# Kernel optimization log

Hardware: AMD Instinct MI355X
Metric: run time of the kernel (lower is better)

Reference implementation:

```python
import jax, jax.numpy as jnp
import numpy as np

N_E = 8192
E_DIM = 256
BETA = 0.25


def setup_inputs() -> dict:
    key = jax.random.key(0)
    k_z, k_w = jax.random.split(key)
    z = jax.random.normal(k_z, (32, E_DIM, 32, 32), dtype=jnp.float32)
    # nn.Embedding weight init: uniform(-1/n_e, 1/n_e)
    W = jax.random.uniform(k_w, (N_E, E_DIM), dtype=jnp.float32,
                           minval=-1.0 / N_E, maxval=1.0 / N_E)
    return {"z": z, "W": W}


def reference(z, W):
    B, C, H, Wd = z.shape
    beta = jnp.float32(BETA)
    z_nhwc = jnp.transpose(z, (0, 2, 3, 1))          # (B,H,W,C)
    zf = z_nhwc.reshape(-1, C)                       # (N,C)
    # squared-distance matrix (N, n_e)
    d = (jnp.sum(zf * zf, axis=1, keepdims=True)
         + jnp.sum(W * W, axis=1)
         - 2.0 * jnp.matmul(zf, W.T))
    idx = jnp.argmin(d, axis=1)                      # (N,)
    # one-hot @ W == gather
    z_q = W[idx].reshape(z_nhwc.shape)               # (B,H,W,C)
    loss = (jnp.mean((jax.lax.stop_gradient(z_q) - z_nhwc) ** 2)
            + beta * jnp.mean((z_q - jax.lax.stop_gradient(z_nhwc)) ** 2))
    # straight-through estimator
    z_q = z_nhwc + jax.lax.stop_gradient(z_q - z_nhwc)
    # codebook usage perplexity
    n = idx.shape[0]
    e_mean = jnp.zeros((N_E,), jnp.float32).at[idx].add(1.0) / n
    perplexity = jnp.exp(-jnp.sum(e_mean * jnp.log(e_mean + 1e-10)))
    z_q = jnp.transpose(z_q, (0, 3, 1, 2))           # back to (B,C,H,W)
    index = idx.reshape(B, H, Wd)
    return z_q, loss, index, perplexity
```

## Files before the change

### kernel.cpp

```cpp
#include <hip/hip_runtime.h>
#include <float.h>
#include <math.h>

#define OUT_LOSS 8388608
#define OUT_IDX  8388609
#define OUT_PERP 8421377

#define WS_ZH    0ull
#define WS_ZL    16777216ull
#define WS_ZT    0ull
#define WS_WH    33554432ull
#define WS_S     37748736ull
#define WS_B     37879808ull
#define WS_MAXW  37912576ull
#define WS_IDX   37912640ull
#define WS_HIST  38043712ull
#define WS_CAND  38076480ull
#define WS_FULL  38469696ull
#define WS_FKEY  38600768ull
#define WS_CNT   38862912ull
#define WS_LOSS  38862920ull

typedef short v8s __attribute__((ext_vector_type(8)));
typedef float v4f __attribute__((ext_vector_type(4)));

__device__ __forceinline__ unsigned short bf16rne(float f) {
  unsigned u = __float_as_uint(f);
  return (unsigned short)((u + 0x7FFFu + ((u >> 16) & 1u)) >> 16);
}
__device__ __forceinline__ float bf16tof(unsigned short h) {
  return __uint_as_float(((unsigned)h) << 16);
}

__device__ __forceinline__ void gl_lds16(const void* g, void* l) {
  __builtin_amdgcn_global_load_lds(
      (const __attribute__((address_space(1))) unsigned int*)g,
      (__attribute__((address_space(3))) unsigned int*)l, 16, 0, 0);
}

__global__ void k_zero(int* __restrict__ hist, unsigned long long* __restrict__ fkey,
                       int* __restrict__ cnt, double* __restrict__ loss,
                       unsigned* __restrict__ maxw) {
  const int i = blockIdx.x * 256 + threadIdx.x;
  if (i < 8192) hist[i] = 0;
  else if (i < 40960) fkey[i - 8192] = ~0ull;
  else if (i == 40960) cnt[0] = 0;
  else if (i == 40961) cnt[1] = 0;
  else if (i == 40962) *loss = 0.0;
  else if (i == 40963) *maxw = 0u;
}

__global__ __launch_bounds__(256) void k_split(const float* __restrict__ W,
                                               unsigned short* __restrict__ Wh) {
  const int u = blockIdx.x * 256 + threadIdx.x;
  const int kc = u >> 15, grp = (u >> 6) & 511, q = (u >> 4) & 3, col = u & 15;
  const int j = grp * 16 + col, k0 = kc * 32 + q * 8;
  const float4 w0 = *(const float4*)(W + (size_t)j * 256 + k0);
  const float4 w1 = *(const float4*)(W + (size_t)j * 256 + k0 + 4);
  const float wv[8] = {w0.x, w0.y, w0.z, w0.w, w1.x, w1.y, w1.z, w1.w};
  unsigned short h[8] __attribute__((aligned(16)));
#pragma unroll
  for (int i = 0; i < 8; ++i) h[i] = bf16rne(wv[i]);
  *(uint4*)(Wh + (size_t)u * 8) = *(const uint4*)h;
}

__global__ __launch_bounds__(256) void k_splitz(const float* __restrict__ z,
    unsigned short* __restrict__ Zh, unsigned short* __restrict__ Zl) {
  const int gt = blockIdx.x * 256 + threadIdx.x;
  const int kc = gt >> 15;
  const int n  = gt & 32767;
  const int b = n >> 10, p = n & 1023;
  const float* zp = z + (size_t)b * 262144 + (size_t)(kc * 32) * 1024 + p;
  unsigned short hh[32] __attribute__((aligned(16)));
  unsigned short ll[32] __attribute__((aligned(16)));
#pragma unroll
  for (int i = 0; i < 32; ++i) {
    const float v = zp[(size_t)i * 1024];
    const unsigned short h = bf16rne(v);
    hh[i] = h;
    ll[i] = bf16rne(__fsub_rn(v, bf16tof(h)));
  }
  const size_t o = (size_t)kc * 1048576 + (size_t)(n >> 4) * 512 + (size_t)(n & 15) * 8;
#pragma unroll
  for (int q = 0; q < 4; ++q) *(uint4*)(Zh + o + q * 128) = *(const uint4*)(hh + q * 8);
#pragma unroll
  for (int q = 0; q < 4; ++q) *(uint4*)(Zl + o + q * 128) = *(const uint4*)(ll + q * 8);
}

__global__ __launch_bounds__(256) void k_zt(const float* __restrict__ z,
                                            float* __restrict__ zT) {
  const int gt = blockIdx.x * 256 + threadIdx.x;
  const int kc = gt >> 15;
  const int n  = gt & 32767;
  const int b = n >> 10, p = n & 1023;
  const float* zp = z + (size_t)b * 262144 + (size_t)(kc * 32) * 1024 + p;
  float v[32] __attribute__((aligned(16)));
#pragma unroll
  for (int i = 0; i < 32; ++i) v[i] = zp[(size_t)i * 1024];
  float* dst = zT + (size_t)n * 256 + kc * 32;
#pragma unroll
  for (int j = 0; j < 8; ++j) *(float4*)(dst + j * 4) = *(const float4*)(v + j * 4);
}

__device__ __forceinline__ float np_sumsq256(const float* __restrict__ base,
                                             const int stride) {
  float h[2];
#pragma unroll
  for (int half = 0; half < 2; ++half) {
    const float* a = base + (size_t)(half * 128) * stride;
    float r[8];
#pragma unroll
    for (int k = 0; k < 8; ++k) { const float v = a[(size_t)k * stride]; r[k] = __fmul_rn(v, v); }
    for (int i = 8; i < 128; i += 8) {
#pragma unroll
      for (int k = 0; k < 8; ++k) {
        const float v = a[(size_t)(i + k) * stride];
        r[k] = __fadd_rn(r[k], __fmul_rn(v, v));
      }
    }
    h[half] = __fadd_rn(
        __fadd_rn(__fadd_rn(r[0], r[1]), __fadd_rn(r[2], r[3])),
        __fadd_rn(__fadd_rn(r[4], r[5]), __fadd_rn(r[6], r[7])));
  }
  return __fadd_rn(h[0], h[1]);
}

__global__ __launch_bounds__(256) void k_sz(const float* __restrict__ z,
                                            float* __restrict__ S) {
  const int n = blockIdx.x * 256 + threadIdx.x;
  S[n] = np_sumsq256(z + (size_t)(n >> 10) * 262144 + (n & 1023), 1024);
}

__global__ __launch_bounds__(256) void k_wsq(const float* __restrict__ W,
                                             float* __restrict__ B,
                                             unsigned* __restrict__ maxw) {
  const int j = blockIdx.x * 256 + threadIdx.x;
  const float b = np_sumsq256(W + (size_t)j * 256, 1);
  B[j] = b;
  atomicMax(maxw, __float_as_uint(b));
}

__device__ __forceinline__ void merge5(float& a1, int& ai1, float& a2, int& ai2,
                                       float& a3, float b1, int bi1, float b2,
                                       int bi2, float b3) {
  const bool t1 = (b1 < a1) || (b1 == a1 && bi1 < ai1);
  const float w2v = t1 ? b2 : a2; const int w2i = t1 ? bi2 : ai2;
  const float w3v = t1 ? b3 : a3;
  const float l1v = t1 ? a1 : b1; const int l1i = t1 ? ai1 : bi1;
  const float l2v = t1 ? a2 : b2;
  const float n1v = t1 ? b1 : a1; const int n1i = t1 ? bi1 : ai1;
  const bool t2 = (w2v < l1v) || (w2v == l1v && w2i < l1i);
  a1 = n1v; ai1 = n1i;
  a2 = t2 ? w2v : l1v; ai2 = t2 ? w2i : l1i;
  a3 = t2 ? fminf(w3v, l1v) : fminf(w2v, l2v);
}

#define AL_OFF 0
#define BQ_OFF 32768
#define B0_OFF 65536
#define B1_OFF 98304
#define B2_OFF 131072
#define SC_OFF 65536
__global__ __launch_bounds__(512, 2) void k_main(
    const unsigned short* __restrict__ Zh, const unsigned short* __restrict__ Zl,
    const unsigned short* __restrict__ Wh, const float* __restrict__ S,
    const float* __restrict__ B, const unsigned* __restrict__ maxw,
    int* __restrict__ idxb, int* __restrict__ cand, int* __restrict__ full,
    int* __restrict__ cnt) {
  extern __shared__ __align__(16) char smem[];
  const int t = threadIdx.x;
  const int w = t >> 6, lane = t & 63, col = lane & 15, q = lane >> 4;
  const int phalf = w >> 2, strip = w & 3;
  const int n0 = blockIdx.x << 6;

  float spx[8];
#pragma unroll
  for (int s = 0; s < 8; ++s)
    spx[s] = S[n0 + phalf * 32 + (s >> 2) * 16 + q * 4 + (s & 3)];

  v8s ah[8][2];
  const size_t abase = (size_t)(n0 >> 4) * 512 + (size_t)lane * 8;
#pragma unroll
  for (int kc = 0; kc < 8; ++kc)
#pragma unroll
    for (int pt = 0; pt < 2; ++pt)
      ah[kc][pt] = *(const v8s*)(Zh + (size_t)kc * 1048576 + abase
                                 + (size_t)(phalf * 2 + pt) * 512);

  {
    const size_t ab = (size_t)w * 1048576 + abase;
    char* dl = smem + AL_OFF + w * 4096;
#pragma unroll
    for (int i = 0; i < 4; ++i) gl_lds16(Zl + ab + (size_t)i * 512, dl + i * 1024);
  }
  {
#pragma unroll
    for (int i = 0; i < 4; ++i)
      gl_lds16(B + (size_t)i * 2048 + (size_t)w * 256 + (size_t)lane * 4,
               smem + BQ_OFF + i * 8192 + w * 1024);
  }
#pragma unroll
  for (int c = 0; c < 2; ++c) {
    const size_t cb = (size_t)(c & 7) * 262144 + (size_t)(w * 4) * 512
                    + (size_t)lane * 8;
    char* d = smem + (c ? B1_OFF : B0_OFF) + (w * 4) * 1024;
#pragma unroll
    for (int i = 0; i < 4; ++i) gl_lds16(Wh + cb + (size_t)i * 512, d + i * 1024);
  }
  asm volatile("s_waitcnt vmcnt(4)" ::: "memory");
  __builtin_amdgcn_s_barrier();
  asm volatile("" ::: "memory");

  float m1[8], m2[8], m3[8]; int i1[8], i2[8];
#pragma unroll
  for (int s = 0; s < 8; ++s) {
    m1[s] = FLT_MAX; m2[s] = FLT_MAX; m3[s] = FLT_MAX;
    i1[s] = 0x7fffffff; i2[s] = 0x7fffffff;
  }

  v4f acc[2][8];
#pragma unroll
  for (int pt = 0; pt < 2; ++pt)
#pragma unroll
    for (int nt = 0; nt < 8; ++nt) acc[pt][nt] = (v4f){0.f, 0.f, 0.f, 0.f};

  char* cur = smem + B0_OFF;
  char* nxt = smem + B1_OFF;
  char* nx2 = smem + B2_OFF;
  const float* bq = (const float*)(smem + BQ_OFF);

  for (int ct = 0; ct < 16; ++ct) {
#pragma unroll
    for (int kc = 0; kc < 8; ++kc) {
      const int it = ct * 8 + kc;
      if (it < 126) {
        const int nc = it + 2;
        const size_t cb = (size_t)(nc & 7) * 262144 + (size_t)(nc >> 3) * 16384
                        + (size_t)(w * 4) * 512 + (size_t)lane * 8;
        char* d = nx2 + (w * 4) * 1024;
#pragma unroll
        for (int i = 0; i < 4; ++i)
          gl_lds16(Wh + cb + (size_t)i * 512, d + i * 1024);
      }
      v8s al[2];
#pragma unroll
      for (int pt = 0; pt < 2; ++pt)
        al[pt] = *(const v8s*)(smem + AL_OFF + kc * 4096
                               + (phalf * 2 + pt) * 1024 + lane * 16);
#pragma unroll
      for (int nt = 0; nt < 8; ++nt) {
        const v8s bh = *(const v8s*)(cur + (strip * 8 + nt) * 1024 + lane * 16);
#pragma unroll
        for (int pt = 0; pt < 2; ++pt) {
          acc[pt][nt] = __builtin_amdgcn_mfma_f32_16x16x32_bf16(ah[kc][pt], bh, acc[pt][nt], 0, 0, 0);
          acc[pt][nt] = __builtin_amdgcn_mfma_f32_16x16x32_bf16(al[pt], bh, acc[pt][nt], 0, 0, 0);
        }
      }
      if (kc == 7) {
#pragma unroll
        for (int nt = 0; nt < 8; ++nt) {
          const int code = ct * 512 + strip * 128 + nt * 16 + col;
          const float bb = bq[code];
#pragma unroll
          for (int pt = 0; pt < 2; ++pt) {
            const v4f a = acc[pt][nt];
#pragma unroll
            for (int r = 0; r < 4; ++r) {
              const int s = pt * 4 + r;
              const float d = __fsub_rn(__fadd_rn(spx[s], bb), __fmul_rn(2.f, a[r]));
              const bool c1 = (d < m1[s]);
              const bool c2 = (d < m2[s]);
              const bool c3 = (d < m3[s]);
              m3[s] = c2 ? m2[s] : (c3 ? d : m3[s]);
              m2[s] = c1 ? m1[s] : (c2 ? d : m2[s]);
              i2[s] = c1 ? i1[s] : (c2 ? code : i2[s]);
              m1[s] = c1 ? d : m1[s];
              i1[s] = c1 ? code : i1[s];
            }
          }
#pragma unroll
          for (int pt = 0; pt < 2; ++pt) acc[pt][nt] = (v4f){0.f, 0.f, 0.f, 0.f};
        }
      }
      if (it < 126) asm volatile("s_waitcnt vmcnt(4)" ::: "memory");
      else          asm volatile("s_waitcnt vmcnt(0)" ::: "memory");
      __builtin_amdgcn_s_barrier();
      asm volatile("" ::: "memory");
      char* tmp = cur; cur = nxt; nxt = nx2; nx2 = tmp;
    }
  }

#pragma unroll
  for (int s = 0; s < 8; ++s) {
    for (int msk = 1; msk < 16; msk <<= 1) {
      const float b1 = __shfl_xor(m1[s], msk, 16);
      const int  bi1 = __shfl_xor(i1[s], msk, 16);
      const float b2 = __shfl_xor(m2[s], msk, 16);
      const int  bi2 = __shfl_xor(i2[s], msk, 16);
      const float b3 = __shfl_xor(m3[s], msk, 16);
      merge5(m1[s], i1[s], m2[s], i2[s], m3[s], b1, bi1, b2, bi2, b3);
    }
  }
  __syncthreads();
  float* sc = (float*)(smem + SC_OFF);
  if (col == 0) {
#pragma unroll
    for (int s = 0; s < 8; ++s) {
      const int px = phalf * 32 + (s >> 2) * 16 + q * 4 + (s & 3);
      const int base = (px * 4 + strip) * 5;
      sc[base]     = m1[s];
      sc[base + 1] = __int_as_float(i1[s]);
      sc[base + 2] = m2[s];
      sc[base + 3] = __int_as_float(i2[s]);
      sc[base + 4] = m3[s];
    }
  }
  __syncthreads();
  if (t < 64) {
    const int base0 = t * 20;
    float A1 = sc[base0], A2 = sc[base0 + 2], A3 = sc[base0 + 4];
    int AI1 = __float_as_int(sc[base0 + 1]), AI2 = __float_as_int(sc[base0 + 3]);
    for (int st = 1; st < 4; ++st) {
      const int base = base0 + st * 5;
      merge5(A1, AI1, A2, AI2, A3, sc[base], __float_as_int(sc[base + 1]),
             sc[base + 2], __float_as_int(sc[base + 3]), sc[base + 4]);
    }
    const int n = n0 + t;
    idxb[n] = AI1;
    const float nw = sqrtf(S[n]) * sqrtf(__uint_as_float(*maxw));
    const float win = 2.0f * (0.001953125f * nw + 1e-6f)
                    + 2.0f * ldexpf(1.0f, ilogbf(fmaxf(A1, 1e-30f)) - 23);
    if (A2 <= A1 + win) {
      if (A3 <= A1 + win) {
        const int p = atomicAdd(&cnt[1], 1);
        full[p] = n;
      } else {
        const int p = atomicAdd(&cnt[0], 1);
        cand[3 * p] = n; cand[3 * p + 1] = AI1; cand[3 * p + 2] = AI2;
      }
    }
  }
}

__global__ __launch_bounds__(256) void k_cand(const float* __restrict__ zT,
    const float* __restrict__ W, const float* __restrict__ S,
    const float* __restrict__ B, const int* __restrict__ cand,
    const int* __restrict__ cnt, int* __restrict__ idxb) {
  const int e = blockIdx.x * 256 + threadIdx.x;
  if (e >= cnt[0]) return;
  const int n = cand[3 * e], ca = cand[3 * e + 1], cb = cand[3 * e + 2];
  const float* zp = zT + (size_t)n * 256;
  const float* wa = W + (size_t)ca * 256;
  const float* wb = W + (size_t)cb * 256;
  float a1 = 0.f, a2 = 0.f;
  for (int c = 0; c < 256; ++c) {
    const float zv = zp[c];
    a1 = __builtin_fmaf(zv, wa[c], a1);
    a2 = __builtin_fmaf(zv, wb[c], a2);
  }
  const float d1 = __fsub_rn(__fadd_rn(S[n], B[ca]), __fmul_rn(2.f, a1));
  const float d2 = __fsub_rn(__fadd_rn(S[n], B[cb]), __fmul_rn(2.f, a2));
  idxb[n] = (d1 < d2) ? ca : ((d2 < d1) ? cb : min(ca, cb));
}

__global__ __launch_bounds__(256) void k_full(const float* __restrict__ zT,
    const float* __restrict__ W, const float* __restrict__ S,
    const float* __restrict__ B, const int* __restrict__ full,
    const int* __restrict__ cnt, unsigned long long* __restrict__ fkey) {
  extern __shared__ __align__(16) char fsm[];
  float* zsf = (float*)fsm;
  float* wt  = (float*)(fsm + 32768);
  float* mv  = (float*)(fsm + 32768 + 32896);
  int*   mi  = (int*)(fsm + 32768 + 32896 + 4224);
  const int t = threadIdx.x;
  const int pg = t & 7, cg = t >> 3;
  const int fN = min(cnt[1], 32768);
  const int units = ((fN + 31) >> 5) << 5;
  for (int e = blockIdx.x; e < units; e += 2048) {
    const int g = e >> 5, tt = e & 31;
    const int c0 = tt << 8;
    __syncthreads();
    {
      const int px = t >> 3, c8 = t & 7;
      const int f = (g << 5) + px;
      const int n = (f < fN) ? full[f] : full[0];
      const float4* src = (const float4*)(zT + (size_t)n * 256 + c8 * 32);
      const int colq = (((px >> 2) ^ c8) << 2) + (px & 3);
#pragma unroll
      for (int j = 0; j < 8; ++j) {
        const float4 v = src[j];
        const int c = c8 * 32 + j * 4;
        zsf[(c    ) * 32 + colq] = v.x;
        zsf[(c + 1) * 32 + colq] = v.y;
        zsf[(c + 2) * 32 + colq] = v.z;
        zsf[(c + 3) * 32 + colq] = v.w;
      }
    }
    float s4[4];
#pragma unroll
    for (int i = 0; i < 4; ++i) {
      const int f = (g << 5) + (pg << 2) + i;
      s4[i] = (f < fN) ? S[full[f]] : 0.f;
    }
    float bm[4]; int bj[4];
#pragma unroll
    for (int i = 0; i < 4; ++i) { bm[i] = FLT_MAX; bj[i] = 0x7fffffff; }
    float acc[4][8];
#pragma unroll
    for (int i = 0; i < 4; ++i)
#pragma unroll
      for (int u = 0; u < 8; ++u) acc[i][u] = 0.f;
    for (int kc = 0; kc < 8; ++kc) {
      const int kb = kc << 5;
      __syncthreads();
#pragma unroll
      for (int p = 0; p < 8; ++p) {
        const int jl = (t >> 3) + (p << 5);
        const float4 wv4 =
            *(const float4*)&W[(size_t)(c0 + jl) * 256 + kb + ((t & 7) << 2)];
        const int k0 = (t & 7) << 2;
        wt[(k0    ) * 257 + jl] = wv4.x;
        wt[(k0 + 1) * 257 + jl] = wv4.y;
        wt[(k0 + 2) * 257 + jl] = wv4.z;
        wt[(k0 + 3) * 257 + jl] = wv4.w;
      }
      __syncthreads();
      const int zq = ((pg ^ kc) & 7) << 2;
      for (int k = 0; k < 32; ++k) {
        const float4 z4 = *(const float4*)&zsf[(kb + k) * 32 + zq];
        const float4 wA = *(const float4*)&wt[k * 257 + (cg << 3)];
        const float4 wB = *(const float4*)&wt[k * 257 + (cg << 3) + 4];
        const float zv[4] = {z4.x, z4.y, z4.z, z4.w};
        const float wv[8] = {wA.x, wA.y, wA.z, wA.w, wB.x, wB.y, wB.z, wB.w};
#pragma unroll
        for (int i = 0; i < 4; ++i)
#pragma unroll
          for (int u = 0; u < 8; ++u)
            acc[i][u] = __builtin_fmaf(zv[i], wv[u], acc[i][u]);
      }
    }
#pragma unroll
    for (int u = 0; u < 8; ++u) {
      const int code = c0 + (cg << 3) + u;
      const float bb = B[code];
#pragma unroll
      for (int i = 0; i < 4; ++i) {
        const float d = __fsub_rn(__fadd_rn(s4[i], bb), __fmul_rn(2.f, acc[i][u]));
        if (d < bm[i]) { bm[i] = d; bj[i] = code; }
      }
    }
    __syncthreads();
#pragma unroll
    for (int i = 0; i < 4; ++i) {
      const int px = (pg << 2) + i;
      mv[px * 33 + cg] = bm[i];
      mi[px * 33 + cg] = bj[i];
    }
    __syncthreads();
    if (t < 32) {
      float m = mv[t * 33]; int j = mi[t * 33];
      for (int c = 1; c < 32; ++c) {
        const float v = mv[t * 33 + c]; const int vi = mi[t * 33 + c];
        if (v < m || (v == m && vi < j)) { m = v; j = vi; }
      }
      const int f = (g << 5) + t;
      if (f < fN) {
        const unsigned long long key =
            (((unsigned long long)__float_as_uint(m)) << 13) | (unsigned)j;
        atomicMin(&fkey[f], key);
      }
    }
  }
}

__global__ __launch_bounds__(256) void k_fullfin(const int* __restrict__ full,
    const int* __restrict__ cnt, const unsigned long long* __restrict__ fkey,
    int* __restrict__ idxb) {
  const int f = blockIdx.x * 256 + threadIdx.x;
  if (f < cnt[1]) idxb[full[f]] = (int)(fkey[f] & 8191ull);
}

__global__ __launch_bounds__(256) void k_zq(const float* __restrict__ z,
    const float* __restrict__ W, const int* __restrict__ idxb,
    float* __restrict__ out, double* __restrict__ loss, int* __restrict__ hist) {
  __shared__ float red[256];
  const int t = threadIdx.x;
  const int tx = t & 63, ty = t >> 6;
  const int n0 = blockIdx.x << 6;
  const int n = n0 + tx;
  const int b = n >> 10;
  const int p = n & 1023;
  const int myidx = idxb[n];
  const float* wrow = W + (size_t)myidx * 256;
  float lsum = 0.f;
#pragma unroll 4
  for (int cc = 0; cc < 64; ++cc) {
    const int c = ty * 64 + cc;
    const float qv = wrow[c];
    const size_t off = (size_t)b * 262144 + (size_t)c * 1024 + p;
    const float zv = z[off];
    const float d = __fsub_rn(qv, zv);
    lsum = __builtin_fmaf(d, d, lsum);
    out[off] = __fadd_rn(zv, d);
  }
  red[t] = lsum;
  __syncthreads();
  for (int o = 128; o > 0; o >>= 1) {
    if (t < o) red[t] += red[t + o];
    __syncthreads();
  }
  if (t == 0) atomicAdd(loss, (double)red[0]);
  if (ty == 0) atomicAdd(&hist[myidx], 1);
  if (ty == 1) out[OUT_IDX + n] = (float)myidx;
}

__global__ void k_final(const int* __restrict__ hist,
                        const double* __restrict__ loss,
                        float* __restrict__ out) {
  __shared__ double sh[256];
  const int t = threadIdx.x;
  double s = 0.0;
  for (int j = t; j < 8192; j += 256) {
    const double e = (double)hist[j] / 32768.0;
    s += e * log(e + 1e-10);
  }
  sh[t] = s;
  __syncthreads();
  for (int off = 128; off > 0; off >>= 1) {
    if (t < off) sh[t] += sh[t + off];
    __syncthreads();
  }
  if (t == 0) {
    out[OUT_PERP] = (float)exp(-sh[0]);
    out[OUT_LOSS] = (float)(1.25 * (*loss) / 8388608.0);
  }
}

extern "C" void kernel_launch(void* const* d_in, const int* in_sizes, int n_in,
                              void* d_out, int out_size, void* d_ws, size_t ws_size,
                              hipStream_t stream) {
  const float* z = (const float*)d_in[0];
  const float* W = (const float*)d_in[1];
  float* out = (float*)d_out;
  char* ws = (char*)d_ws;
  unsigned short* Zh = (unsigned short*)(ws + WS_ZH);
  unsigned short* Zl = (unsigned short*)(ws + WS_ZL);
  unsigned short* Wh = (unsigned short*)(ws + WS_WH);
  float*  zT   = (float*)(ws + WS_ZT);
  float*  S    = (float*)(ws + WS_S);
  float*  B    = (float*)(ws + WS_B);
  unsigned* maxw = (unsigned*)(ws + WS_MAXW);
  int*    idxb = (int*)(ws + WS_IDX);
  int*    hist = (int*)(ws + WS_HIST);
  int*    cand = (int*)(ws + WS_CAND);
  int*    full = (int*)(ws + WS_FULL);
  unsigned long long* fkey = (unsigned long long*)(ws + WS_FKEY);
  int*    cnt  = (int*)(ws + WS_CNT);
  double* loss = (double*)(ws + WS_LOSS);

  hipLaunchKernelGGL(k_zero,    dim3(161),  dim3(256), 0, stream, hist, fkey, cnt, loss, maxw);
  hipLaunchKernelGGL(k_split,   dim3(1024), dim3(256), 0, stream, W, Wh);
  hipLaunchKernelGGL(k_splitz,  dim3(1024), dim3(256), 0, stream, z, Zh, Zl);
  hipLaunchKernelGGL(k_sz,      dim3(128),  dim3(256), 0, stream, z, S);
  hipLaunchKernelGGL(k_wsq,     dim3(32),   dim3(256), 0, stream, W, B, maxw);
  hipLaunchKernelGGL(k_main,    dim3(512),  dim3(512), 163840, stream,
                     Zh, Zl, Wh, S, B, maxw, idxb, cand, full, cnt);
  hipLaunchKernelGGL(k_zt,      dim3(1024), dim3(256), 0, stream, z, zT);
  hipLaunchKernelGGL(k_cand,    dim3(128),  dim3(256), 0, stream, zT, W, S, B, cand, cnt, idxb);
  hipLaunchKernelGGL(k_full,    dim3(2048), dim3(256), 74112, stream, zT, W, S, B, full, cnt, fkey);
  hipLaunchKernelGGL(k_fullfin, dim3(128),  dim3(256), 0, stream, full, cnt, fkey, idxb);
  hipLaunchKernelGGL(k_zq,      dim3(512),  dim3(256), 0, stream, z, W, idxb, out, loss, hist);
  hipLaunchKernelGGL(k_final,   dim3(1),    dim3(256), 0, stream, hist, loss, out);
}
```

Before: 822.3 us.

## Add third bf16 split term for W to tighten candidate window

Splits the codebook into high and low bf16 parts and adds a third MFMA (z_hi x W_lo) per tile. This makes the main distance GEMM nearly fp32-accurate, so the tie window shrinks and fewer points go to the exact candidate and full recheck passes. In exchange the main loop does about 50% more MFMA work and loads twice the W bytes per step. The triple-buffered prefetch with vmcnt waits becomes double buffering with a full __syncthreads after every k-chunk, and B is now read from global memory instead of LDS.

```diff
diff --git a/kernel.cpp b/kernel.cpp
--- a/kernel.cpp
+++ b/kernel.cpp
@@ -20,6 +20,7 @@
 #define WS_FKEY  38600768ull
 #define WS_CNT   38862912ull
 #define WS_LOSS  38862920ull
+#define WS_WL    38866944ull
 
 typedef short v8s __attribute__((ext_vector_type(8)));
 typedef float v4f __attribute__((ext_vector_type(4)));
@@ -51,7 +52,8 @@
 }
 
 __global__ __launch_bounds__(256) void k_split(const float* __restrict__ W,
-                                               unsigned short* __restrict__ Wh) {
+                                               unsigned short* __restrict__ Wh,
+                                               unsigned short* __restrict__ Wl) {
   const int u = blockIdx.x * 256 + threadIdx.x;
   const int kc = u >> 15, grp = (u >> 6) & 511, q = (u >> 4) & 3, col = u & 15;
   const int j = grp * 16 + col, k0 = kc * 32 + q * 8;
@@ -59,9 +61,14 @@
   const float4 w1 = *(const float4*)(W + (size_t)j * 256 + k0 + 4);
   const float wv[8] = {w0.x, w0.y, w0.z, w0.w, w1.x, w1.y, w1.z, w1.w};
   unsigned short h[8] __attribute__((aligned(16)));
-#pragma unroll
-  for (int i = 0; i < 8; ++i) h[i] = bf16rne(wv[i]);
+  unsigned short l[8] __attribute__((aligned(16)));
+#pragma unroll
+  for (int i = 0; i < 8; ++i) {
+    h[i] = bf16rne(wv[i]);
+    l[i] = bf16rne(__fsub_rn(wv[i], bf16tof(h[i])));
+  }
   *(uint4*)(Wh + (size_t)u * 8) = *(const uint4*)h;
+  *(uint4*)(Wl + (size_t)u * 8) = *(const uint4*)l;
 }
 
 __global__ __launch_bounds__(256) void k_splitz(const float* __restrict__ z,
@@ -155,18 +162,19 @@
   a3 = t2 ? fminf(w3v, l1v) : fminf(w2v, l2v);
 }
 
-#define AL_OFF 0
-#define BQ_OFF 32768
-#define B0_OFF 65536
-#define B1_OFF 98304
-#define B2_OFF 131072
-#define SC_OFF 65536
+#define AL_OFF   0
+#define BH0_OFF  32768
+#define BH1_OFF  65536
+#define BL0_OFF  98304
+#define BL1_OFF  131072
+#define SC_OFF   32768
+#define SMEM_SZ  163840
 __global__ __launch_bounds__(512, 2) void k_main(
     const unsigned short* __restrict__ Zh, const unsigned short* __restrict__ Zl,
-    const unsigned short* __restrict__ Wh, const float* __restrict__ S,
-    const float* __restrict__ B, const unsigned* __restrict__ maxw,
-    int* __restrict__ idxb, int* __restrict__ cand, int* __restrict__ full,
-    int* __restrict__ cnt) {
+    const unsigned short* __restrict__ Wh, const unsigned short* __restrict__ Wl,
+    const float* __restrict__ S, const float* __restrict__ B,
+    const unsigned* __restrict__ maxw, int* __restrict__ idxb,
+    int* __restrict__ cand, int* __restrict__ full, int* __restrict__ cnt) {
   extern __shared__ __align__(16) char smem[];
   const int t = threadIdx.x;
   const int w = t >> 6, lane = t & 63, col = lane & 15, q = lane >> 4;
@@ -194,22 +202,15 @@
     for (int i = 0; i < 4; ++i) gl_lds16(Zl + ab + (size_t)i * 512, dl + i * 1024);
   }
   {
+    const size_t bb = (size_t)(w * 4) * 512 + (size_t)lane * 8;
 #pragma unroll
     for (int i = 0; i < 4; ++i)
-      gl_lds16(B + (size_t)i * 2048 + (size_t)w * 256 + (size_t)lane * 4,
-               smem + BQ_OFF + i * 8192 + w * 1024);
-  }
-#pragma unroll
-  for (int c = 0; c < 2; ++c) {
-    const size_t cb = (size_t)(c & 7) * 262144 + (size_t)(w * 4) * 512
-                    + (size_t)lane * 8;
-    char* d = smem + (c ? B1_OFF : B0_OFF) + (w * 4) * 1024;
-#pragma unroll
-    for (int i = 0; i < 4; ++i) gl_lds16(Wh + cb + (size_t)i * 512, d + i * 1024);
-  }
-  asm volatile("s_waitcnt vmcnt(4)" ::: "memory");
-  __builtin_amdgcn_s_barrier();
-  asm volatile("" ::: "memory");
+      gl_lds16(Wh + bb + (size_t)i * 512, smem + BH0_OFF + (w * 4 + i) * 1024);
+#pragma unroll
+    for (int i = 0; i < 4; ++i)
+      gl_lds16(Wl + bb + (size_t)i * 512, smem + BL0_OFF + (w * 4 + i) * 1024);
+  }
+  __syncthreads();
 
   float m1[8], m2[8], m3[8]; int i1[8], i2[8];
 #pragma unroll
@@ -224,24 +225,25 @@
 #pragma unroll
     for (int nt = 0; nt < 8; ++nt) acc[pt][nt] = (v4f){0.f, 0.f, 0.f, 0.f};
 
-  char* cur = smem + B0_OFF;
-  char* nxt = smem + B1_OFF;
-  char* nx2 = smem + B2_OFF;
-  const float* bq = (const float*)(smem + BQ_OFF);
-
   for (int ct = 0; ct < 16; ++ct) {
 #pragma unroll
     for (int kc = 0; kc < 8; ++kc) {
       const int it = ct * 8 + kc;
-      if (it < 126) {
-        const int nc = it + 2;
+      if (it < 127) {
+        const int nc = it + 1;
         const size_t cb = (size_t)(nc & 7) * 262144 + (size_t)(nc >> 3) * 16384
                         + (size_t)(w * 4) * 512 + (size_t)lane * 8;
-        char* d = nx2 + (w * 4) * 1024;
+        char* nh = smem + ((nc & 1) ? BH1_OFF : BH0_OFF) + (w * 4) * 1024;
+        char* nl = smem + ((nc & 1) ? BL1_OFF : BL0_OFF) + (w * 4) * 1024;
 #pragma unroll
         for (int i = 0; i < 4; ++i)
-          gl_lds16(Wh + cb + (size_t)i * 512, d + i * 1024);
-      }
+          gl_lds16(Wh + cb + (size_t)i * 512, nh + i * 1024);
+#pragma unroll
+        for (int i = 0; i < 4; ++i)
+          gl_lds16(Wl + cb + (size_t)i * 512, nl + i * 1024);
+      }
+      const char* bhb = smem + ((it & 1) ? BH1_OFF : BH0_OFF);
+      const char* blb = smem + ((it & 1) ? BL1_OFF : BL0_OFF);
       v8s al[2];
 #pragma unroll
       for (int pt = 0; pt < 2; ++pt)
@@ -249,18 +251,21 @@
                                + (phalf * 2 + pt) * 1024 + lane * 16);
 #pragma unroll
       for (int nt = 0; nt < 8; ++nt) {
-        const v8s bh = *(const v8s*)(cur + (strip * 8 + nt) * 1024 + lane * 16);
+        const v8s bh = *(const v8s*)(bhb + (strip * 8 + nt) * 1024 + lane * 16);
+        const v8s bl = *(const v8s*)(blb + (strip * 8 + nt) * 1024 + lane * 16);
 #pragma unroll
         for (int pt = 0; pt < 2; ++pt) {
           acc[pt][nt] = __builtin_amdgcn_mfma_f32_16x16x32_bf16(ah[kc][pt], bh, acc[pt][nt], 0, 0, 0);
           acc[pt][nt] = __builtin_amdgcn_mfma_f32_16x16x32_bf16(al[pt], bh, acc[pt][nt], 0, 0, 0);
+          acc[pt][nt] = __builtin_amdgcn_mfma_f32_16x16x32_bf16(ah[kc][pt], bl, acc[pt][nt], 0, 0, 0);
         }
       }
+      __syncthreads();
       if (kc == 7) {
 #pragma unroll
         for (int nt = 0; nt < 8; ++nt) {
           const int code = ct * 512 + strip * 128 + nt * 16 + col;
-          const float bb = bq[code];
+          const float bb = B[code];
 #pragma unroll
           for (int pt = 0; pt < 2; ++pt) {
             const v4f a = acc[pt][nt];
@@ -282,11 +287,6 @@
           for (int pt = 0; pt < 2; ++pt) acc[pt][nt] = (v4f){0.f, 0.f, 0.f, 0.f};
         }
       }
-      if (it < 126) asm volatile("s_waitcnt vmcnt(4)" ::: "memory");
-      else          asm volatile("s_waitcnt vmcnt(0)" ::: "memory");
-      __builtin_amdgcn_s_barrier();
-      asm volatile("" ::: "memory");
-      char* tmp = cur; cur = nxt; nxt = nx2; nx2 = tmp;
     }
   }
 
@@ -328,7 +328,7 @@
     const int n = n0 + t;
     idxb[n] = AI1;
     const float nw = sqrtf(S[n]) * sqrtf(__uint_as_float(*maxw));
-    const float win = 2.0f * (0.001953125f * nw + 1e-6f)
+    const float win = 2.0f * (1.52587890625e-05f * nw + 1e-6f)
                     + 2.0f * ldexpf(1.0f, ilogbf(fmaxf(A1, 1e-30f)) - 23);
     if (A2 <= A1 + win) {
       if (A3 <= A1 + win) {
@@ -546,6 +546,7 @@
   unsigned short* Zh = (unsigned short*)(ws + WS_ZH);
   unsigned short* Zl = (unsigned short*)(ws + WS_ZL);
   unsigned short* Wh = (unsigned short*)(ws + WS_WH);
+  unsigned short* Wl = (unsigned short*)(ws + WS_WL);
   float*  zT   = (float*)(ws + WS_ZT);
   float*  S    = (float*)(ws + WS_S);
   float*  B    = (float*)(ws + WS_B);
@@ -559,12 +560,12 @@
   double* loss = (double*)(ws + WS_LOSS);
 
   hipLaunchKernelGGL(k_zero,    dim3(161),  dim3(256), 0, stream, hist, fkey, cnt, loss, maxw);
-  hipLaunchKernelGGL(k_split,   dim3(1024), dim3(256), 0, stream, W, Wh);
+  hipLaunchKernelGGL(k_split,   dim3(1024), dim3(256), 0, stream, W, Wh, Wl);
   hipLaunchKernelGGL(k_splitz,  dim3(1024), dim3(256), 0, stream, z, Zh, Zl);
   hipLaunchKernelGGL(k_sz,      dim3(128),  dim3(256), 0, stream, z, S);
   hipLaunchKernelGGL(k_wsq,     dim3(32),   dim3(256), 0, stream, W, B, maxw);
-  hipLaunchKernelGGL(k_main,    dim3(512),  dim3(512), 163840, stream,
-                     Zh, Zl, Wh, S, B, maxw, idxb, cand, full, cnt);
+  hipLaunchKernelGGL(k_main,    dim3(512),  dim3(512), SMEM_SZ, stream,
+                     Zh, Zl, Wh, Wl, S, B, maxw, idxb, cand, full, cnt);
   hipLaunchKernelGGL(k_zt,      dim3(1024), dim3(256), 0, stream, z, zT);
   hipLaunchKernelGGL(k_cand,    dim3(128),  dim3(256), 0, stream, zT, W, S, B, cand, cnt, idxb);
   hipLaunchKernelGGL(k_full,    dim3(2048), dim3(256), 74112, stream, zT, W, S, B, full, cnt, fkey);
```

New measurement: 834.9 us. No clear change (+1.5%).
